# Kernel tuning notes

Hardware: AMD Instinct MI355X
Metric: run time of the kernel (lower is better)

The kernel has to match this reference:

```python
import jax, jax.numpy as jnp
import numpy as np

B, N, FD, HD, G = 32, 512, 768, 384, 3
ALPHA = 0.2  # LeakyReLU slope
NEG = -9e15


def layer_norm(x, g, b, eps=1e-5):
    m = jnp.mean(x, axis=-1, keepdims=True)
    v = jnp.var(x, axis=-1, keepdims=True)
    return (x - m) / jnp.sqrt(v + eps) * g + b


def gat_layer(x, adj, W, a):
    # x: [B,N,FD], adj: [N,N], W: [FD,HD], a: [2*HD]
    h = jnp.einsum('bnf,fd->bnd', x, W)  # [B,N,HD]
    # concat score decomposes: e_ij = lrelu(h_i . a[:HD] + h_j . a[HD:])
    e1 = h @ a[:HD]   # [B,N]
    e2 = h @ a[HD:]   # [B,N]
    e = jax.nn.leaky_relu(e1[:, :, None] + e2[:, None, :], ALPHA)  # [B,N,N]
    e = jnp.where(adj[None] > 0, e, NEG)
    att = jax.nn.softmax(e, axis=2)  # masked softmax over neighbors
    h_prime = jnp.einsum('bij,bjd->bid', att, h)
    return jax.nn.elu(h_prime)  # concat=True -> ELU


def setup_inputs() -> dict:
    key = jax.random.key(0)
    ks = jax.random.split(key, 10)
    s = 0.05
    return {
        'x': jax.random.normal(ks[0], (B, N, FD), jnp.float32),
        'adj': jax.random.randint(ks[1], (G, N, N), 0, 2),
        'W': jax.random.normal(ks[2], (G, FD, HD), jnp.float32) * s,
        'a': jax.random.normal(ks[3], (G, 2 * HD), jnp.float32) * s,
        'log_unc': jnp.zeros((G,), jnp.float32),
        'gate_w': jax.random.normal(ks[4], (FD, G), jnp.float32) * s,
        'gate_b': jnp.zeros((G,), jnp.float32),
        'ln1_g': jnp.ones((HD,), jnp.float32),
        'ln1_b': jnp.zeros((HD,), jnp.float32),
        'w1': jax.random.normal(ks[5], (HD, HD), jnp.float32) * s,
        'b1': jnp.zeros((HD,), jnp.float32),
        'w2': jax.random.normal(ks[6], (HD, FD), jnp.float32) * s,
        'b2': jnp.zeros((FD,), jnp.float32),
        'ln2_g': jnp.ones((FD,), jnp.float32),
        'ln2_b': jnp.zeros((FD,), jnp.float32),
    }


def reference(x, adj, W, a, log_unc, gate_w, gate_b, ln1_g, ln1_b,
              w1, b1, w2, b2, ln2_g, ln2_b):
    # global (uncertainty) weights
    unc = jnp.exp(log_unc)
    attw = jax.nn.softmax(1.0 / (unc + 1e-8))  # [G]
    # content gates from batch-averaged features
    avg = jnp.mean(x, axis=0)                          # [N,FD]
    cg = jax.nn.softmax(avg @ gate_w + gate_b, axis=-1)  # [N,G]
    # per-graph GAT + LayerNorm, vmapped over the G graphs
    gouts = jax.vmap(lambda ad, Wi, ai: layer_norm(gat_layer(x, ad, Wi, ai), ln1_g, ln1_b))(adj, W, a)  # [G,B,N,HD]
    weights = 0.7 * attw[:, None, None, None] + 0.3 * cg.T[:, None, :, None]  # [G,1|B,N,1]
    fused = jnp.sum(weights * gouts, axis=0)  # [B,N,HD]
    # output projection + LayerNorm
    proj = jax.nn.relu(fused @ w1 + b1) @ w2 + b2
    proj = layer_norm(proj, ln2_g, ln2_b)
    # residual gate
    gv = jax.nn.sigmoid(jnp.sum(proj * x, axis=-1, keepdims=True) / np.sqrt(FD).astype(np.float32))
    return gv * x + (1.0 - gv) * proj
```

## Files before the change

### kernel.cpp

```cpp
#include <hip/hip_runtime.h>

typedef unsigned short ushort_t;
typedef unsigned int uint_t;
typedef __bf16 bf16x8 __attribute__((ext_vector_type(8)));
typedef float f32x4 __attribute__((ext_vector_type(4)));
typedef unsigned int u32x4 __attribute__((ext_vector_type(4)));
typedef unsigned short u16x4 __attribute__((ext_vector_type(4)));

#define B_SZ 32
#define N_SZ 512
#define FD_SZ 768
#define HD_SZ 384
#define G_SZ 3
#define M_SZ (B_SZ * N_SZ)
#define ALPHA_LR 0.2f
#define NEGV -9.0e15f
#define VTILE (HD_SZ * 32)

__device__ __forceinline__ float bflo(uint_t u) { return __uint_as_float(u << 16); }
__device__ __forceinline__ float bfhi(uint_t u) { return __uint_as_float(u & 0xffff0000u); }
__device__ __forceinline__ float bf2f(ushort_t u) { return __uint_as_float(((uint_t)u) << 16); }
__device__ __forceinline__ ushort_t f2bf(float f) {
  uint_t x = __float_as_uint(f);
  return (ushort_t)((x + 0x7fffu + ((x >> 16) & 1u)) >> 16);
}
__device__ __forceinline__ u32x4 pack8(f32x4 lo, f32x4 hi) {
  union { ushort_t us[8]; u32x4 v; } pk;
  pk.us[0] = f2bf(lo.x); pk.us[1] = f2bf(lo.y); pk.us[2] = f2bf(lo.z); pk.us[3] = f2bf(lo.w);
  pk.us[4] = f2bf(hi.x); pk.us[5] = f2bf(hi.y); pk.us[6] = f2bf(hi.z); pk.us[7] = f2bf(hi.w);
  return pk.v;
}

__global__ __launch_bounds__(256) void transpose_f2b(
    const float* __restrict__ src, ushort_t* __restrict__ dst, int R, int C) {
  size_t total = (size_t)R * C;
  size_t base = (size_t)blockIdx.z * total;
  size_t i = (size_t)blockIdx.x * 256 + threadIdx.x;
  if (i < total) {
    int r = (int)(i / C), c = (int)(i % C);
    dst[base + (size_t)c * R + r] = f2bf(src[base + i]);
  }
}

__global__ __launch_bounds__(256) void gate_kernel(
    const float* __restrict__ x, const float* __restrict__ gate_w,
    const float* __restrict__ gate_b, float* __restrict__ cg) {
  int n = blockIdx.x;
  int tid = threadIdx.x;
  float a0 = 0.f, a1 = 0.f, a2 = 0.f;
  for (int f = tid; f < FD_SZ; f += 256) {
    float s = 0.f;
#pragma unroll
    for (int b = 0; b < B_SZ; b++) s += x[((size_t)b * N_SZ + n) * FD_SZ + f];
    float avg = s * (1.0f / B_SZ);
    a0 += avg * gate_w[f * 3 + 0];
    a1 += avg * gate_w[f * 3 + 1];
    a2 += avg * gate_w[f * 3 + 2];
  }
  for (int m = 1; m < 64; m <<= 1) {
    a0 += __shfl_xor(a0, m, 64);
    a1 += __shfl_xor(a1, m, 64);
    a2 += __shfl_xor(a2, m, 64);
  }
  __shared__ float red[3][4];
  int wave = tid >> 6, lane = tid & 63;
  if (lane == 0) { red[0][wave] = a0; red[1][wave] = a1; red[2][wave] = a2; }
  __syncthreads();
  if (tid == 0) {
    float l0 = red[0][0] + red[0][1] + red[0][2] + red[0][3] + gate_b[0];
    float l1 = red[1][0] + red[1][1] + red[1][2] + red[1][3] + gate_b[1];
    float l2 = red[2][0] + red[2][1] + red[2][2] + red[2][3] + gate_b[2];
    float mx = fmaxf(l0, fmaxf(l1, l2));
    float e0 = __expf(l0 - mx), e1 = __expf(l1 - mx), e2 = __expf(l2 - mx);
    float inv = 1.0f / (e0 + e1 + e2);
    cg[n * 3 + 0] = e0 * inv;
    cg[n * 3 + 1] = e1 * inv;
    cg[n * 3 + 2] = e2 * inv;
  }
}

template <bool AF32, bool RELU, bool OUTBF16, bool HASBIAS, bool VFOUT>
__global__ __launch_bounds__(256) void gemm_kernel(
    const void* __restrict__ Av, size_t strideA,
    const ushort_t* __restrict__ Bt, size_t strideB,
    const float* __restrict__ bias,
    void* __restrict__ Cv, size_t strideC,
    int M, int K, int Nc) {
  __shared__ __attribute__((aligned(16))) ushort_t As[128 * 32];
  __shared__ __attribute__((aligned(16))) ushort_t Bs[128 * 32];
  int tid = threadIdx.x, wave = tid >> 6, lane = tid & 63;
  int m0 = blockIdx.y * 128, n0 = blockIdx.x * 128;
  const float* Abf32 = (const float*)Av + (size_t)blockIdx.z * strideA;
  const ushort_t* Abb16 = (const ushort_t*)Av + (size_t)blockIdx.z * strideA;
  const ushort_t* Bb = Bt + (size_t)blockIdx.z * strideB;

  f32x4 acc[4][4];
  f32x4 z4 = {0.f, 0.f, 0.f, 0.f};
#pragma unroll
  for (int i = 0; i < 4; i++)
#pragma unroll
    for (int j = 0; j < 4; j++) acc[i][j] = z4;

  int wm = (wave & 1) * 64, wn = (wave >> 1) * 64;
  int srow = lane >> 2, schk = (lane & 3) * 8;

  for (int kt = 0; kt < K; kt += 32) {
    u32x4 av[2], bv[2];
#pragma unroll
    for (int i = 0; i < 2; i++) {
      int row = m0 + wave * 32 + i * 16 + srow;
      if (AF32) {
        const float* ap = Abf32 + (size_t)row * K + kt + schk;
        f32x4 lo = *(const f32x4*)ap;
        f32x4 hi = *(const f32x4*)(ap + 4);
        av[i] = pack8(lo, hi);
      } else {
        av[i] = *(const u32x4*)(Abb16 + (size_t)row * K + kt + schk);
      }
      bv[i] = *(const u32x4*)(Bb + (size_t)(n0 + wave * 32 + i * 16 + srow) * K + kt + schk);
    }
    __syncthreads();
#pragma unroll
    for (int i = 0; i < 2; i++) {
      int rowBase = wave * 32 + i * 16;
      *(u32x4*)(As + rowBase * 32 + lane * 8) = av[i];
      *(u32x4*)(Bs + rowBase * 32 + lane * 8) = bv[i];
    }
    __syncthreads();
    bf16x8 af[4], bfr[4];
#pragma unroll
    for (int t = 0; t < 4; t++) {
      af[t] = *(const bf16x8*)(As + (wm + t * 16 + (lane & 15)) * 32 + (lane >> 4) * 8);
      bfr[t] = *(const bf16x8*)(Bs + (wn + t * 16 + (lane & 15)) * 32 + (lane >> 4) * 8);
    }
#pragma unroll
    for (int mt = 0; mt < 4; mt++)
#pragma unroll
      for (int nt = 0; nt < 4; nt++)
        acc[mt][nt] = __builtin_amdgcn_mfma_f32_16x16x32_bf16(af[mt], bfr[nt], acc[mt][nt], 0, 0, 0);
  }

  if (VFOUT) {
#pragma unroll
    for (int mt = 0; mt < 4; mt++) {
#pragma unroll
      for (int nt = 0; nt < 4; nt++) {
        int d = n0 + wn + nt * 16 + (lane & 15);
        int gm = m0 + wm + mt * 16 + (lane >> 4) * 4;
        int b = gm >> 9, jt = (gm >> 5) & 15, j2 = gm & 31;
        u16x4 pk;
#pragma unroll
        for (int r2 = 0; r2 < 4; r2++) pk[r2] = f2bf(acc[mt][nt][r2]);
        size_t off = ((size_t)((blockIdx.z * B_SZ + b) * 16 + jt)) * VTILE + (size_t)d * 32 + j2;
        *(u16x4*)((ushort_t*)Cv + off) = pk;
      }
    }
  } else {
#pragma unroll
    for (int mt = 0; mt < 4; mt++) {
#pragma unroll
      for (int nt = 0; nt < 4; nt++) {
        int gn = n0 + wn + nt * 16 + (lane & 15);
        float bvs = HASBIAS ? bias[gn] : 0.f;
#pragma unroll
        for (int r2 = 0; r2 < 4; r2++) {
          int gm = m0 + wm + mt * 16 + (lane >> 4) * 4 + r2;
          float v = acc[mt][nt][r2] + bvs;
          if (RELU) v = v > 0.f ? v : 0.f;
          size_t off = (size_t)blockIdx.z * strideC + (size_t)gm * Nc + gn;
          if (OUTBF16) ((ushort_t*)Cv)[off] = f2bf(v);
          else ((float*)Cv)[off] = v;
        }
      }
    }
  }
}

__global__ __launch_bounds__(256) void e12_kernel(
    const ushort_t* __restrict__ vf, const float* __restrict__ a,
    float* __restrict__ e1, float* __restrict__ e2) {
  __shared__ float a1s[HD_SZ], a2s[HD_SZ];
  int g = blockIdx.y;
  int tid = threadIdx.x;
  for (int i = tid; i < HD_SZ; i += 256) {
    a1s[i] = a[g * 2 * HD_SZ + i];
    a2s[i] = a[g * 2 * HD_SZ + HD_SZ + i];
  }
  __syncthreads();
  int m = blockIdx.x * 256 + tid;
  int b = m >> 9, jt = (m >> 5) & 15, j2 = m & 31;
  const ushort_t* col = vf + ((size_t)((g * B_SZ + b) * 16 + jt)) * VTILE + j2;
  float s1 = 0.f, s2 = 0.f;
  for (int d = 0; d < HD_SZ; d++) {
    float h = bf2f(col[d * 32]);
    s1 += h * a1s[d];
    s2 += h * a2s[d];
  }
  e1[(size_t)g * M_SZ + m] = s1;
  e2[(size_t)g * M_SZ + m] = s2;
}

__global__ __launch_bounds__(256) void attn_kernel(
    const int* __restrict__ adj, const ushort_t* __restrict__ vf,
    const float* __restrict__ e1, const float* __restrict__ e2,
    const float* __restrict__ cg, const float* __restrict__ log_unc,
    const float* __restrict__ ln1g, const float* __restrict__ ln1b,
    ushort_t* __restrict__ fusedbf) {
  __shared__ __attribute__((aligned(16))) ushort_t Pb[16][520];
  __shared__ float e2s[512];
  __shared__ float e1r[16];
  __shared__ float lng[HD_SZ], lnb[HD_SZ];
  __shared__ float cgr[16][3];
  __shared__ float s1s[16][4], s2s[16][4];

  int tid = threadIdx.x, wave = tid >> 6, lane = tid & 63;
  int quad = lane >> 4, l15 = lane & 15;
  int b = blockIdx.y, i0 = blockIdx.x * 16;

  float iv0 = 1.f / (__expf(log_unc[0]) + 1e-8f);
  float iv1 = 1.f / (__expf(log_unc[1]) + 1e-8f);
  float iv2 = 1.f / (__expf(log_unc[2]) + 1e-8f);
  float mxa = fmaxf(iv0, fmaxf(iv1, iv2));
  float w0 = __expf(iv0 - mxa), w1 = __expf(iv1 - mxa), w2 = __expf(iv2 - mxa);
  float wsum = 1.f / (w0 + w1 + w2);
  float attw[3] = {w0 * wsum, w1 * wsum, w2 * wsum};

  for (int idx = tid; idx < HD_SZ; idx += 256) {
    lng[idx] = ln1g[idx];
    lnb[idx] = ln1b[idx];
  }
  if (tid < 48) cgr[tid / 3][tid % 3] = cg[(i0 + tid / 3) * 3 + tid % 3];

  float facc[24];
#pragma unroll
  for (int t = 0; t < 24; t++) facc[t] = 0.f;

  for (int g = 0; g < G_SZ; g++) {
    __syncthreads();
    if (tid < 16) e1r[tid] = e1[((size_t)g * B_SZ + b) * N_SZ + i0 + tid];
    for (int idx = tid; idx < N_SZ; idx += 256)
      e2s[idx] = e2[((size_t)g * B_SZ + b) * N_SZ + idx];
    __syncthreads();

#pragma unroll
    for (int rr = 0; rr < 4; rr++) {
      int rw = wave * 4 + rr;
      const int* arow = adj + ((size_t)g * N_SZ + i0 + rw) * N_SZ;
      float e1v = e1r[rw];
      float sv[8];
      float m = -3.0e38f;
#pragma unroll
      for (int jj = 0; jj < 8; jj++) {
        int j = lane + jj * 64;
        float s = e1v + e2s[j];
        s = s > 0.f ? s : ALPHA_LR * s;
        s = arow[j] > 0 ? s : NEGV;
        sv[jj] = s;
        m = fmaxf(m, s);
      }
      for (int msk = 1; msk < 64; msk <<= 1) m = fmaxf(m, __shfl_xor(m, msk, 64));
      float sum = 0.f;
#pragma unroll
      for (int jj = 0; jj < 8; jj++) {
        float e = __expf(sv[jj] - m);
        sv[jj] = e;
        sum += e;
      }
      for (int msk = 1; msk < 64; msk <<= 1) sum += __shfl_xor(sum, msk, 64);
      float inv = 1.0f / sum;
#pragma unroll
      for (int jj = 0; jj < 8; jj++) Pb[rw][lane + jj * 64] = f2bf(sv[jj] * inv);
    }
    __syncthreads();

    f32x4 acc[6];
    f32x4 z4 = {0.f, 0.f, 0.f, 0.f};
#pragma unroll
    for (int t = 0; t < 6; t++) acc[t] = z4;
    const ushort_t* vbase = vf + ((size_t)(g * B_SZ + b) * 16) * VTILE;
    for (int j0 = 0; j0 < N_SZ; j0 += 32) {
      bf16x8 af = *(const bf16x8*)(&Pb[l15][j0 + quad * 8]);
      const ushort_t* vtile = vbase + (size_t)(j0 >> 5) * VTILE;
#pragma unroll
      for (int t = 0; t < 6; t++) {
        bf16x8 bf = *(const bf16x8*)(vtile + (wave * 96 + t * 16 + l15) * 32 + quad * 8);
        acc[t] = __builtin_amdgcn_mfma_f32_16x16x32_bf16(af, bf, acc[t], 0, 0, 0);
      }
    }

    float o[24];
    float ps1[4] = {0.f, 0.f, 0.f, 0.f}, ps2[4] = {0.f, 0.f, 0.f, 0.f};
#pragma unroll
    for (int t = 0; t < 6; t++)
#pragma unroll
      for (int r = 0; r < 4; r++) {
        float v = acc[t][r];
        v = v > 0.f ? v : __expf(v) - 1.f;
        o[t * 4 + r] = v;
        ps1[r] += v;
        ps2[r] += v * v;
      }
#pragma unroll
    for (int msk = 1; msk < 16; msk <<= 1) {
#pragma unroll
      for (int r = 0; r < 4; r++) {
        ps1[r] += __shfl_xor(ps1[r], msk, 64);
        ps2[r] += __shfl_xor(ps2[r], msk, 64);
      }
    }
    if (l15 == 0) {
#pragma unroll
      for (int r = 0; r < 4; r++) {
        s1s[quad * 4 + r][wave] = ps1[r];
        s2s[quad * 4 + r][wave] = ps2[r];
      }
    }
    __syncthreads();
#pragma unroll
    for (int r = 0; r < 4; r++) {
      int row = quad * 4 + r;
      float S1 = s1s[row][0] + s1s[row][1] + s1s[row][2] + s1s[row][3];
      float S2 = s2s[row][0] + s2s[row][1] + s2s[row][2] + s2s[row][3];
      float mean = S1 * (1.f / HD_SZ);
      float var = S2 * (1.f / HD_SZ) - mean * mean;
      float rs = rsqrtf(var + 1e-5f);
      float wgt = 0.7f * attw[g] + 0.3f * cgr[row][g];
#pragma unroll
      for (int t = 0; t < 6; t++) {
        int d = wave * 96 + t * 16 + l15;
        facc[t * 4 + r] += wgt * ((o[t * 4 + r] - mean) * rs * lng[d] + lnb[d]);
      }
    }
  }
#pragma unroll
  for (int r = 0; r < 4; r++) {
    size_t rowo = ((size_t)b * N_SZ + i0 + quad * 4 + r) * HD_SZ;
#pragma unroll
    for (int t = 0; t < 6; t++)
      fusedbf[rowo + wave * 96 + t * 16 + l15] = f2bf(facc[t * 4 + r]);
  }
}

__global__ __launch_bounds__(256) void final_kernel(
    const ushort_t* __restrict__ projbf, const float* __restrict__ x,
    const float* __restrict__ ln2g, const float* __restrict__ ln2b,
    float* __restrict__ out) {
  int row = blockIdx.x;
  int tid = threadIdx.x, wave = tid >> 6, lane = tid & 63;
  const ushort_t* pr = projbf + (size_t)row * FD_SZ;
  const float* xr = x + (size_t)row * FD_SZ;
  float v[3], xv[3];
  float s1 = 0.f, s2 = 0.f;
#pragma unroll
  for (int k = 0; k < 3; k++) {
    int c = tid + k * 256;
    v[k] = bf2f(pr[c]);
    xv[k] = xr[c];
    s1 += v[k];
    s2 += v[k] * v[k];
  }
  for (int m = 1; m < 64; m <<= 1) {
    s1 += __shfl_xor(s1, m, 64);
    s2 += __shfl_xor(s2, m, 64);
  }
  __shared__ float rs1[4], rs2[4], rdt[4];
  if (lane == 0) { rs1[wave] = s1; rs2[wave] = s2; }
  __syncthreads();
  s1 = rs1[0] + rs1[1] + rs1[2] + rs1[3];
  s2 = rs2[0] + rs2[1] + rs2[2] + rs2[3];
  float mean = s1 * (1.f / FD_SZ);
  float var = s2 * (1.f / FD_SZ) - mean * mean;
  float rstd = rsqrtf(var + 1e-5f);
  float dot = 0.f;
  float pn[3];
#pragma unroll
  for (int k = 0; k < 3; k++) {
    int c = tid + k * 256;
    pn[k] = (v[k] - mean) * rstd * ln2g[c] + ln2b[c];
    dot += pn[k] * xv[k];
  }
  for (int m = 1; m < 64; m <<= 1) dot += __shfl_xor(dot, m, 64);
  if (lane == 0) rdt[wave] = dot;
  __syncthreads();
  dot = rdt[0] + rdt[1] + rdt[2] + rdt[3];
  float gv = 1.f / (1.f + __expf(-dot * (1.0f / 27.712812921102035f)));
#pragma unroll
  for (int k = 0; k < 3; k++) {
    int c = tid + k * 256;
    out[(size_t)row * FD_SZ + c] = gv * xv[k] + (1.f - gv) * pn[k];
  }
}

extern "C" void kernel_launch(void* const* d_in, const int* in_sizes, int n_in,
                              void* d_out, int out_size, void* d_ws, size_t ws_size,
                              hipStream_t stream) {
  (void)in_sizes; (void)n_in; (void)out_size; (void)ws_size;
  const float* x = (const float*)d_in[0];
  const int* adj = (const int*)d_in[1];
  const float* W = (const float*)d_in[2];
  const float* a = (const float*)d_in[3];
  const float* log_unc = (const float*)d_in[4];
  const float* gate_w = (const float*)d_in[5];
  const float* gate_b = (const float*)d_in[6];
  const float* ln1g = (const float*)d_in[7];
  const float* ln1b = (const float*)d_in[8];
  const float* w1 = (const float*)d_in[9];
  const float* b1 = (const float*)d_in[10];
  const float* w2 = (const float*)d_in[11];
  const float* b2 = (const float*)d_in[12];
  const float* ln2g = (const float*)d_in[13];
  const float* ln2b = (const float*)d_in[14];

  char* ws = (char*)d_ws;
  ushort_t* Wt      = (ushort_t*)(ws + 0);
  ushort_t* w1t     = (ushort_t*)(ws + 1769472);
  ushort_t* w2t     = (ushort_t*)(ws + 2064384);
  float*    cg      = (float*)(ws + 2654208);
  float*    e1      = (float*)(ws + 2660352);
  float*    e2      = (float*)(ws + 2856960);
  ushort_t* fusedbf = (ushort_t*)(ws + 3053568);
  ushort_t* vf      = (ushort_t*)(ws + 15636480);
  ushort_t* t1bf    = (ushort_t*)(ws + 15636480);
  ushort_t* projbf  = (ushort_t*)(ws + 28219392);

  transpose_f2b<<<dim3(1152, 1, 3), 256, 0, stream>>>(W, Wt, FD_SZ, HD_SZ);
  transpose_f2b<<<dim3(576, 1, 1), 256, 0, stream>>>(w1, w1t, HD_SZ, HD_SZ);
  transpose_f2b<<<dim3(1152, 1, 1), 256, 0, stream>>>(w2, w2t, HD_SZ, FD_SZ);

  gate_kernel<<<dim3(N_SZ), 256, 0, stream>>>(x, gate_w, gate_b, cg);

  gemm_kernel<true, false, true, false, true><<<dim3(3, 128, 3), 256, 0, stream>>>(
      x, 0, Wt, (size_t)HD_SZ * FD_SZ, nullptr, vf, 0,
      M_SZ, FD_SZ, HD_SZ);

  e12_kernel<<<dim3(M_SZ / 256, G_SZ), 256, 0, stream>>>(vf, a, e1, e2);

  attn_kernel<<<dim3(N_SZ / 16, B_SZ), 256, 0, stream>>>(
      adj, vf, e1, e2, cg, log_unc, ln1g, ln1b, fusedbf);

  gemm_kernel<false, true, true, true, false><<<dim3(3, 128, 1), 256, 0, stream>>>(
      fusedbf, 0, w1t, 0, b1, t1bf, 0, M_SZ, HD_SZ, HD_SZ);
  gemm_kernel<false, false, true, true, false><<<dim3(6, 128, 1), 256, 0, stream>>>(
      t1bf, 0, w2t, 0, b2, projbf, 0, M_SZ, HD_SZ, FD_SZ);

  final_kernel<<<dim3(M_SZ), 256, 0, stream>>>(projbf, x, ln2g, ln2b, (float*)d_out);
}
```

Baseline: 368.8 us.

## Bit-pack adjacency masks and widen attention blocks to eight waves

```diff
diff --git a/kernel.cpp b/kernel.cpp
--- a/kernel.cpp
+++ b/kernel.cpp
@@ -40,6 +40,14 @@
     int r = (int)(i / C), c = (int)(i % C);
     dst[base + (size_t)c * R + r] = f2bf(src[base + i]);
   }
+}
+
+__global__ __launch_bounds__(256) void pack_adj(
+    const int* __restrict__ adj, uint_t* __restrict__ am) {
+  size_t i = (size_t)blockIdx.x * 256 + threadIdx.x;
+  unsigned long long mask = __ballot(adj[i] != 0);
+  int lane = threadIdx.x & 63;
+  if ((lane & 31) == 0) am[i >> 5] = (uint_t)(mask >> (lane & 32));
 }
 
 __global__ __launch_bounds__(256) void gate_kernel(
@@ -200,8 +208,8 @@
   e2[(size_t)g * M_SZ + m] = s2;
 }
 
-__global__ __launch_bounds__(256) void attn_kernel(
-    const int* __restrict__ adj, const ushort_t* __restrict__ vf,
+__global__ __launch_bounds__(512, 8) void attn_kernel(
+    const uint_t* __restrict__ adjm, const ushort_t* __restrict__ vf,
     const float* __restrict__ e1, const float* __restrict__ e2,
     const float* __restrict__ cg, const float* __restrict__ log_unc,
     const float* __restrict__ ln1g, const float* __restrict__ ln1b,
@@ -209,9 +217,10 @@
   __shared__ __attribute__((aligned(16))) ushort_t Pb[16][520];
   __shared__ float e2s[512];
   __shared__ float e1r[16];
+  __shared__ uint_t amS[16][16];
   __shared__ float lng[HD_SZ], lnb[HD_SZ];
   __shared__ float cgr[16][3];
-  __shared__ float s1s[16][4], s2s[16][4];
+  __shared__ float s1s[16][8], s2s[16][8];
 
   int tid = threadIdx.x, wave = tid >> 6, lane = tid & 63;
   int quad = lane >> 4, l15 = lane & 15;
@@ -225,27 +234,28 @@
   float wsum = 1.f / (w0 + w1 + w2);
   float attw[3] = {w0 * wsum, w1 * wsum, w2 * wsum};
 
-  for (int idx = tid; idx < HD_SZ; idx += 256) {
+  for (int idx = tid; idx < HD_SZ; idx += 512) {
     lng[idx] = ln1g[idx];
     lnb[idx] = ln1b[idx];
   }
   if (tid < 48) cgr[tid / 3][tid % 3] = cg[(i0 + tid / 3) * 3 + tid % 3];
 
-  float facc[24];
-#pragma unroll
-  for (int t = 0; t < 24; t++) facc[t] = 0.f;
+  float facc[12];
+#pragma unroll
+  for (int t = 0; t < 12; t++) facc[t] = 0.f;
 
   for (int g = 0; g < G_SZ; g++) {
     __syncthreads();
     if (tid < 16) e1r[tid] = e1[((size_t)g * B_SZ + b) * N_SZ + i0 + tid];
-    for (int idx = tid; idx < N_SZ; idx += 256)
+    if (tid < 256)
+      amS[tid >> 4][tid & 15] = adjm[((size_t)g * N_SZ + i0 + (tid >> 4)) * 16 + (tid & 15)];
+    for (int idx = tid; idx < N_SZ; idx += 512)
       e2s[idx] = e2[((size_t)g * B_SZ + b) * N_SZ + idx];
     __syncthreads();
 
 #pragma unroll
-    for (int rr = 0; rr < 4; rr++) {
-      int rw = wave * 4 + rr;
-      const int* arow = adj + ((size_t)g * N_SZ + i0 + rw) * N_SZ;
+    for (int rr = 0; rr < 2; rr++) {
+      int rw = wave * 2 + rr;
       float e1v = e1r[rw];
       float sv[8];
       float m = -3.0e38f;
@@ -254,7 +264,8 @@
         int j = lane + jj * 64;
         float s = e1v + e2s[j];
         s = s > 0.f ? s : ALPHA_LR * s;
-        s = arow[j] > 0 ? s : NEGV;
+        uint_t mw = amS[rw][(lane >> 5) + jj * 2];
+        s = ((mw >> (j & 31)) & 1u) ? s : NEGV;
         sv[jj] = s;
         m = fmaxf(m, s);
       }
@@ -273,25 +284,25 @@
     }
     __syncthreads();
 
-    f32x4 acc[6];
+    f32x4 acc[3];
     f32x4 z4 = {0.f, 0.f, 0.f, 0.f};
 #pragma unroll
-    for (int t = 0; t < 6; t++) acc[t] = z4;
+    for (int t = 0; t < 3; t++) acc[t] = z4;
     const ushort_t* vbase = vf + ((size_t)(g * B_SZ + b) * 16) * VTILE;
     for (int j0 = 0; j0 < N_SZ; j0 += 32) {
       bf16x8 af = *(const bf16x8*)(&Pb[l15][j0 + quad * 8]);
       const ushort_t* vtile = vbase + (size_t)(j0 >> 5) * VTILE;
 #pragma unroll
-      for (int t = 0; t < 6; t++) {
-        bf16x8 bf = *(const bf16x8*)(vtile + (wave * 96 + t * 16 + l15) * 32 + quad * 8);
+      for (int t = 0; t < 3; t++) {
+        bf16x8 bf = *(const bf16x8*)(vtile + (wave * 48 + t * 16 + l15) * 32 + quad * 8);
         acc[t] = __builtin_amdgcn_mfma_f32_16x16x32_bf16(af, bf, acc[t], 0, 0, 0);
       }
     }
 
-    float o[24];
+    float o[12];
     float ps1[4] = {0.f, 0.f, 0.f, 0.f}, ps2[4] = {0.f, 0.f, 0.f, 0.f};
 #pragma unroll
-    for (int t = 0; t < 6; t++)
+    for (int t = 0; t < 3; t++)
 #pragma unroll
       for (int r = 0; r < 4; r++) {
         float v = acc[t][r];
@@ -319,15 +330,19 @@
 #pragma unroll
     for (int r = 0; r < 4; r++) {
       int row = quad * 4 + r;
-      float S1 = s1s[row][0] + s1s[row][1] + s1s[row][2] + s1s[row][3];
-      float S2 = s2s[row][0] + s2s[row][1] + s2s[row][2] + s2s[row][3];
+      float S1 = 0.f, S2 = 0.f;
+#pragma unroll
+      for (int w = 0; w < 8; w++) {
+        S1 += s1s[row][w];
+        S2 += s2s[row][w];
+      }
       float mean = S1 * (1.f / HD_SZ);
       float var = S2 * (1.f / HD_SZ) - mean * mean;
       float rs = rsqrtf(var + 1e-5f);
       float wgt = 0.7f * attw[g] + 0.3f * cgr[row][g];
 #pragma unroll
-      for (int t = 0; t < 6; t++) {
-        int d = wave * 96 + t * 16 + l15;
+      for (int t = 0; t < 3; t++) {
+        int d = wave * 48 + t * 16 + l15;
         facc[t * 4 + r] += wgt * ((o[t * 4 + r] - mean) * rs * lng[d] + lnb[d]);
       }
     }
@@ -336,8 +351,8 @@
   for (int r = 0; r < 4; r++) {
     size_t rowo = ((size_t)b * N_SZ + i0 + quad * 4 + r) * HD_SZ;
 #pragma unroll
-    for (int t = 0; t < 6; t++)
-      fusedbf[rowo + wave * 96 + t * 16 + l15] = f2bf(facc[t * 4 + r]);
+    for (int t = 0; t < 3; t++)
+      fusedbf[rowo + wave * 48 + t * 16 + l15] = f2bf(facc[t * 4 + r]);
   }
 }
 
@@ -413,6 +428,7 @@
 
   char* ws = (char*)d_ws;
   ushort_t* Wt      = (ushort_t*)(ws + 0);
+  uint_t*   adjm    = (uint_t*)(ws + 0);
   ushort_t* w1t     = (ushort_t*)(ws + 1769472);
   ushort_t* w2t     = (ushort_t*)(ws + 2064384);
   float*    cg      = (float*)(ws + 2654208);
@@ -433,10 +449,12 @@
       x, 0, Wt, (size_t)HD_SZ * FD_SZ, nullptr, vf, 0,
       M_SZ, FD_SZ, HD_SZ);
 
+  pack_adj<<<dim3((G_SZ * N_SZ * N_SZ) / 256), 256, 0, stream>>>(adj, adjm);
+
   e12_kernel<<<dim3(M_SZ / 256, G_SZ), 256, 0, stream>>>(vf, a, e1, e2);
 
-  attn_kernel<<<dim3(N_SZ / 16, B_SZ), 256, 0, stream>>>(
-      adj, vf, e1, e2, cg, log_unc, ln1g, ln1b, fusedbf);
+  attn_kernel<<<dim3(N_SZ / 16, B_SZ), 512, 0, stream>>>(
+      adjm, vf, e1, e2, cg, log_unc, ln1g, ln1b, fusedbf);
 
   gemm_kernel<false, true, true, true, false><<<dim3(3, 128, 1), 256, 0, stream>>>(
       fusedbf, 0, w1t, 0, b1, t1bf, 0, M_SZ, HD_SZ, HD_SZ);
```

After: 383.9 us. 4.1% more time.
